# Performance work log

Hardware: AMD Instinct MI355X
Metric: run time of the kernel (lower is better)

The kernel has to match this reference:

```python
import jax, jax.numpy as jnp
import numpy as np

BN_EPS = 1e-5
NEG_SLOPE = 0.2

def _avgpool2(x):
    B, C, H, W = x.shape
    return x.reshape(B, C, H // 2, 2, W // 2, 2).mean(axis=(3, 5))

def _conv1x1(x, w, b):
    # x: [B,C,H,W], w: [O,C], b: [O]
    return jnp.einsum('bchw,oc->bohw', x, w) + b[None, :, None, None]

def _bilinear_resize(x, out_h, out_w):
    # PyTorch F.interpolate(mode='bilinear', align_corners=False) semantics
    B, C, h, w = x.shape
    ys = jnp.maximum((jnp.arange(out_h, dtype=jnp.float32) + 0.5) * (h / out_h) - 0.5, 0.0)
    xs = jnp.maximum((jnp.arange(out_w, dtype=jnp.float32) + 0.5) * (w / out_w) - 0.5, 0.0)
    y0 = jnp.floor(ys).astype(jnp.int32); x0 = jnp.floor(xs).astype(jnp.int32)
    wy = (ys - y0.astype(jnp.float32)).astype(x.dtype)
    wx = (xs - x0.astype(jnp.float32)).astype(x.dtype)
    y1 = jnp.minimum(y0 + 1, h - 1); x1 = jnp.minimum(x0 + 1, w - 1)
    rows = x[:, :, y0, :] * (1.0 - wy)[None, None, :, None] + x[:, :, y1, :] * wy[None, None, :, None]
    out = rows[:, :, :, x0] * (1.0 - wx)[None, None, None, :] + rows[:, :, :, x1] * wx[None, None, None, :]
    return out

def setup_inputs() -> dict:
    key = jax.random.key(0)
    ks = jax.random.split(key, 16)
    B, Cin, Hid, Cout, H, W = 8, 64, 64, 64, 128, 128
    s = 0.05
    return {
        'rgb': jax.random.normal(ks[0], (B, Cin, H, W), dtype=jnp.float32),
        'freq': jax.random.normal(ks[1], (B, Cin, H, W), dtype=jnp.float32),
        'w_q': jax.random.normal(ks[2], (Hid, Cin), dtype=jnp.float32) * s,
        'b_q': jax.random.normal(ks[3], (Hid,), dtype=jnp.float32) * s,
        'w_k': jax.random.normal(ks[4], (Hid, Cin), dtype=jnp.float32) * s,
        'b_k': jax.random.normal(ks[5], (Hid,), dtype=jnp.float32) * s,
        'w_v': jax.random.normal(ks[6], (Hid, Cin), dtype=jnp.float32) * s,
        'b_v': jax.random.normal(ks[7], (Hid,), dtype=jnp.float32) * s,
        'w_o': jax.random.normal(ks[8], (Cout, Hid), dtype=jnp.float32) * s,
        'b_o': jax.random.normal(ks[9], (Cout,), dtype=jnp.float32) * s,
        'bn_gamma': jnp.ones((Cout,), dtype=jnp.float32),
        'bn_beta': jnp.zeros((Cout,), dtype=jnp.float32),
        'bn_mean': jax.random.normal(ks[10], (Cout,), dtype=jnp.float32) * s,
        'bn_var': jax.random.uniform(ks[11], (Cout,), dtype=jnp.float32, minval=0.5, maxval=1.5),
    }

def reference(rgb, freq, w_q, b_q, w_k, b_k, w_v, b_v, w_o, b_o, bn_gamma, bn_beta, bn_mean, bn_var):
    B, C, H, W = rgb.shape
    rgb_ds = _avgpool2(rgb)
    freq_ds = _avgpool2(freq)
    hd, wd = rgb_ds.shape[2], rgb_ds.shape[3]
    hid = w_q.shape[0]
    scale = hid ** (-0.5)
    # 1x1 conv QKV projections, flatten spatial dims to tokens N = hd*wd
    q = _conv1x1(rgb_ds, w_q, b_q).reshape(B, hid, hd * wd)   # [B,hid,N]
    k = _conv1x1(freq_ds, w_k, b_k).reshape(B, hid, hd * wd)  # [B,hid,N]
    v = _conv1x1(freq_ds, w_v, b_v).reshape(B, hid, hd * wd)  # [B,hid,N]
    attn = jax.nn.softmax(jnp.einsum('bcn,bcm->bnm', q, k) * scale, axis=-1)  # [B,N,N]
    z = jnp.einsum('bnm,bcm->bcn', attn, v).reshape(B, hid, hd, wd)
    z = _bilinear_resize(z, H, W)
    y = _conv1x1(z, w_o, b_o)
    # inference-mode BatchNorm fused as affine
    inv = bn_gamma / jnp.sqrt(bn_var + BN_EPS)
    y = (y - bn_mean[None, :, None, None]) * inv[None, :, None, None] + bn_beta[None, :, None, None]
    y = jnp.where(y >= 0, y, NEG_SLOPE * y)  # LeakyReLU(0.2)
    return rgb + y
```

## Files before the change

### kernel.cpp

```cpp
#include <hip/hip_runtime.h>
#include <hip/hip_bf16.h>

typedef unsigned short u16;
typedef unsigned int   u32;
typedef __attribute__((ext_vector_type(8))) short bf16x8;
typedef __attribute__((ext_vector_type(4))) float f32x4;

__device__ __forceinline__ u16 f2bf(float f) {
  u32 u = __float_as_uint(f);
  u32 r = u + 0x7fffu + ((u >> 16) & 1u);
  return (u16)(r >> 16);
}
__device__ __forceinline__ float bflo(u32 u) { return __uint_as_float(u << 16); }
__device__ __forceinline__ float bfhi(u32 u) { return __uint_as_float(u & 0xffff0000u); }
__device__ __forceinline__ u32 packhi(float a, float b) {
  return __builtin_amdgcn_perm(__float_as_uint(b), __float_as_uint(a), 0x07060302u);
}

__global__ __launch_bounds__(256, 4) void k_qkv(
    const float* __restrict__ rgb, const float* __restrict__ freq,
    const float* __restrict__ wq, const float* __restrict__ bq,
    const float* __restrict__ wk, const float* __restrict__ bk,
    const float* __restrict__ wv, const float* __restrict__ bv,
    u16* __restrict__ Qo, u16* __restrict__ Ko, u16* __restrict__ Vo)
{
  __shared__ __align__(16) u16 sm[3 * 4608];
  u16* X  = sm;
  u16* W0 = sm + 4608;
  u16* W1 = sm + 9216;

  const int t    = threadIdx.x;
  const int side = blockIdx.x & 1;
  const int seg  = blockIdx.x >> 1;
  const int idx0 = seg * 64;
  const int bb   = idx0 >> 12;
  const int n0   = idx0 & 4095;
  const int h    = n0 >> 6;
  const float* src = side ? freq : rgb;

  const size_t sbase = (size_t)bb * 64 * 16384 + (size_t)(2 * h) * 128;
  for (int i = 0; i < 2; ++i) {
    int cell = i * 256 + t;
    int tok  = cell & 63;
    int grp  = cell >> 6;
    const float* p0 = src + sbase + 2 * tok + (size_t)(grp * 8) * 16384;
    u32 pk[4];
#pragma unroll
    for (int cc = 0; cc < 8; cc += 2) {
      const float* pa = p0 + (size_t)cc * 16384;
      float2 a0 = *(const float2*)pa;
      float2 a1 = *(const float2*)(pa + 128);
      float v0 = 0.25f * ((a0.x + a0.y) + (a1.x + a1.y));
      const float* pb = pa + 16384;
      float2 b0 = *(const float2*)pb;
      float2 b1 = *(const float2*)(pb + 128);
      float v1 = 0.25f * ((b0.x + b0.y) + (b1.x + b1.y));
      pk[cc >> 1] = (u32)f2bf(v0) | ((u32)f2bf(v1) << 16);
    }
    uint4 q4; q4.x = pk[0]; q4.y = pk[1]; q4.z = pk[2]; q4.w = pk[3];
    *(uint4*)&X[tok * 72 + grp * 8] = q4;
  }
  {
    const int o = t >> 2, c0 = (t & 3) << 4;
    const float4* p4 = (const float4*)((side ? wk : wq) + o * 64 + c0);
    float4 f0 = p4[0], f1 = p4[1], f2 = p4[2], f3 = p4[3];
    uint4 qa, qb;
    qa.x = (u32)f2bf(f0.x) | ((u32)f2bf(f0.y) << 16);
    qa.y = (u32)f2bf(f0.z) | ((u32)f2bf(f0.w) << 16);
    qa.z = (u32)f2bf(f1.x) | ((u32)f2bf(f1.y) << 16);
    qa.w = (u32)f2bf(f1.z) | ((u32)f2bf(f1.w) << 16);
    qb.x = (u32)f2bf(f2.x) | ((u32)f2bf(f2.y) << 16);
    qb.y = (u32)f2bf(f2.z) | ((u32)f2bf(f2.w) << 16);
    qb.z = (u32)f2bf(f3.x) | ((u32)f2bf(f3.y) << 16);
    qb.w = (u32)f2bf(f3.z) | ((u32)f2bf(f3.w) << 16);
    *(uint4*)&W0[o * 72 + c0] = qa;
    *(uint4*)&W0[o * 72 + c0 + 8] = qb;
    if (side) {
      const float4* v4 = (const float4*)(wv + o * 64 + c0);
      float4 g0 = v4[0], g1 = v4[1], g2 = v4[2], g3 = v4[3];
      qa.x = (u32)f2bf(g0.x) | ((u32)f2bf(g0.y) << 16);
      qa.y = (u32)f2bf(g0.z) | ((u32)f2bf(g0.w) << 16);
      qa.z = (u32)f2bf(g1.x) | ((u32)f2bf(g1.y) << 16);
      qa.w = (u32)f2bf(g1.z) | ((u32)f2bf(g1.w) << 16);
      qb.x = (u32)f2bf(g2.x) | ((u32)f2bf(g2.y) << 16);
      qb.y = (u32)f2bf(g2.z) | ((u32)f2bf(g2.w) << 16);
      qb.z = (u32)f2bf(g3.x) | ((u32)f2bf(g3.y) << 16);
      qb.w = (u32)f2bf(g3.z) | ((u32)f2bf(g3.w) << 16);
      *(uint4*)&W1[o * 72 + c0] = qa;
      *(uint4*)&W1[o * 72 + c0 + 8] = qb;
    }
  }
  __syncthreads();

  const int lane = t & 63, w = t >> 6;
  const int l15 = lane & 15, qd = lane >> 4;
  const int tb = w * 16;

  bf16x8 af0 = *(const bf16x8*)&X[(tb + l15) * 72 + qd * 8];
  bf16x8 af1 = *(const bf16x8*)&X[(tb + l15) * 72 + 32 + qd * 8];

  f32x4 acc[4];
#pragma unroll
  for (int nt = 0; nt < 4; ++nt) {
    bf16x8 b0 = *(const bf16x8*)&W0[(nt * 16 + l15) * 72 + qd * 8];
    bf16x8 b1 = *(const bf16x8*)&W0[(nt * 16 + l15) * 72 + 32 + qd * 8];
    f32x4 a = {0.f, 0.f, 0.f, 0.f};
    a = __builtin_amdgcn_mfma_f32_16x16x32_bf16(af0, b0, a, 0, 0, 0);
    a = __builtin_amdgcn_mfma_f32_16x16x32_bf16(af1, b1, a, 0, 0, 0);
    acc[nt] = a;
  }
  {
    const float* bias0 = side ? bk : bq;
    const float sc = side ? 1.f : 0.18033688f;
    u16* dst0 = side ? Ko : Qo;
#pragma unroll
    for (int nt = 0; nt < 4; ++nt) {
      float bia = bias0[nt * 16 + l15];
#pragma unroll
      for (int e = 0; e < 4; ++e) {
        int tok = idx0 + tb + qd * 4 + e;
        dst0[(size_t)tok * 64 + nt * 16 + l15] = f2bf((acc[nt][e] + bia) * sc);
      }
    }
  }

  if (side) {
    f32x4 accv[4];
#pragma unroll
    for (int ct = 0; ct < 4; ++ct) {
      bf16x8 a0 = *(const bf16x8*)&W1[(ct * 16 + l15) * 72 + qd * 8];
      bf16x8 a1 = *(const bf16x8*)&W1[(ct * 16 + l15) * 72 + 32 + qd * 8];
      f32x4 a = {0.f, 0.f, 0.f, 0.f};
      a = __builtin_amdgcn_mfma_f32_16x16x32_bf16(a0, af0, a, 0, 0, 0);
      a = __builtin_amdgcn_mfma_f32_16x16x32_bf16(a1, af1, a, 0, 0, 0);
      accv[ct] = a;
    }
#pragma unroll
    for (int ct = 0; ct < 4; ++ct) {
#pragma unroll
      for (int e = 0; e < 4; ++e) {
        int c = ct * 16 + qd * 4 + e;
        float v = accv[ct][e] + bv[c];
        Vo[((size_t)(bb * 64 + c)) * 4096 + n0 + tb + l15] = f2bf(v);
      }
    }
  }
}

__global__ __launch_bounds__(256, 2) void k_attn(
    const u16* __restrict__ Qg, const u16* __restrict__ Kg,
    const u16* __restrict__ Vg,
    const float* __restrict__ wo, const float* __restrict__ bo,
    const float* __restrict__ gam, const float* __restrict__ bet,
    const float* __restrict__ mean, const float* __restrict__ var,
    u16* __restrict__ Ya)
{
  __shared__ __align__(16) u16 Pb[4 * 4608];
  __shared__ __align__(16) u16 Wl[4608];
  __shared__ __align__(16) u16 Zc[4608];
  __shared__ float lb[256];

  const int b  = blockIdx.x;
  const int q0 = blockIdx.y * 64;
  const int t  = threadIdx.x;
  const int lane = t & 63, w = t >> 6;
  const int l15 = lane & 15, qd = lane >> 4;
  u16* P = Pb + w * 4608;

  {
    const int o = t >> 2, c0 = (t & 3) << 4;
    const float4* p4 = (const float4*)(wo + o * 64 + c0);
    float4 f0 = p4[0], f1 = p4[1], f2 = p4[2], f3 = p4[3];
    uint4 qa, qb;
    qa.x = (u32)f2bf(f0.x) | ((u32)f2bf(f0.y) << 16);
    qa.y = (u32)f2bf(f0.z) | ((u32)f2bf(f0.w) << 16);
    qa.z = (u32)f2bf(f1.x) | ((u32)f2bf(f1.y) << 16);
    qa.w = (u32)f2bf(f1.z) | ((u32)f2bf(f1.w) << 16);
    qb.x = (u32)f2bf(f2.x) | ((u32)f2bf(f2.y) << 16);
    qb.y = (u32)f2bf(f2.z) | ((u32)f2bf(f2.w) << 16);
    qb.z = (u32)f2bf(f3.x) | ((u32)f2bf(f3.y) << 16);
    qb.w = (u32)f2bf(f3.z) | ((u32)f2bf(f3.w) << 16);
    *(uint4*)&Wl[o * 72 + c0] = qa;
    *(uint4*)&Wl[o * 72 + c0 + 8] = qb;
  }

  bf16x8 qf[4][2];
#pragma unroll
  for (int qt = 0; qt < 4; ++qt) {
    const u16* p = Qg + ((size_t)(b * 4096 + q0 + qt * 16 + l15)) * 64 + qd * 8;
    qf[qt][0] = *(const bf16x8*)p;
    qf[qt][1] = *(const bf16x8*)(p + 32);
  }

  f32x4 zacc[4][4];
#pragma unroll
  for (int i = 0; i < 4; ++i)
#pragma unroll
    for (int j = 0; j < 4; ++j) {
      f32x4 z = {0.f, 0.f, 0.f, 0.f};
      zacc[i][j] = z;
    }
  float lacc[4] = {0.f, 0.f, 0.f, 0.f};

  for (int tile = 0; tile < 16; ++tile) {
    const int n0 = w * 1024 + tile * 64;

    bf16x8 kf[4][2], vf[4][2];
#pragma unroll
    for (int mt = 0; mt < 4; ++mt) {
      const u16* p = Kg + ((size_t)(b * 4096 + n0 + mt * 16 + l15)) * 64 + qd * 8;
      kf[mt][0] = *(const bf16x8*)p;
      kf[mt][1] = *(const bf16x8*)(p + 32);
    }
#pragma unroll
    for (int ct = 0; ct < 4; ++ct) {
      const u16* p = Vg + ((size_t)(b * 64 + ct * 16 + l15)) * 4096 + n0 + qd * 8;
      vf[ct][0] = *(const bf16x8*)p;
      vf[ct][1] = *(const bf16x8*)(p + 32);
    }

#pragma unroll
    for (int qt = 0; qt < 4; ++qt) {
#pragma unroll
      for (int mt = 0; mt < 4; ++mt) {
        f32x4 a = {0.f, 0.f, 0.f, 0.f};
        __builtin_amdgcn_s_setprio(1);
        a = __builtin_amdgcn_mfma_f32_16x16x32_bf16(kf[mt][0], qf[qt][0], a, 0, 0, 0);
        a = __builtin_amdgcn_mfma_f32_16x16x32_bf16(kf[mt][1], qf[qt][1], a, 0, 0, 0);
        __builtin_amdgcn_s_setprio(0);
        float p0 = __builtin_amdgcn_exp2f(a[0]);
        float p1 = __builtin_amdgcn_exp2f(a[1]);
        float p2 = __builtin_amdgcn_exp2f(a[2]);
        float p3 = __builtin_amdgcn_exp2f(a[3]);
        lacc[qt] += (p0 + p1) + (p2 + p3);
        uint2 pw;
        pw.x = packhi(p0, p1);
        pw.y = packhi(p2, p3);
        *(uint2*)&P[(qt * 16 + l15) * 72 + mt * 16 + qd * 4] = pw;
      }
    }
#pragma unroll
    for (int qt = 0; qt < 4; ++qt) {
      bf16x8 pf0 = *(const bf16x8*)&P[(qt * 16 + l15) * 72 + qd * 8];
      bf16x8 pf1 = *(const bf16x8*)&P[(qt * 16 + l15) * 72 + 32 + qd * 8];
      __builtin_amdgcn_s_setprio(1);
#pragma unroll
      for (int ct = 0; ct < 4; ++ct) {
        zacc[ct][qt] = __builtin_amdgcn_mfma_f32_16x16x32_bf16(vf[ct][0], pf0, zacc[ct][qt], 0, 0, 0);
        zacc[ct][qt] = __builtin_amdgcn_mfma_f32_16x16x32_bf16(vf[ct][1], pf1, zacc[ct][qt], 0, 0, 0);
      }
      __builtin_amdgcn_s_setprio(0);
    }
  }

#pragma unroll
  for (int qt = 0; qt < 4; ++qt) {
    float l = lacc[qt];
    l += __shfl_xor(l, 16);
    l += __shfl_xor(l, 32);
    lb[w * 64 + qt * 16 + l15] = l;
  }
#pragma unroll
  for (int qt = 0; qt < 4; ++qt)
#pragma unroll
    for (int ct = 0; ct < 4; ++ct) {
      uint2 pw;
      pw.x = packhi(zacc[ct][qt][0], zacc[ct][qt][1]);
      pw.y = packhi(zacc[ct][qt][2], zacc[ct][qt][3]);
      *(uint2*)&P[(qt * 16 + l15) * 72 + ct * 16 + qd * 4] = pw;
    }
  __syncthreads();

  {
    const u32* Pu = (const u32*)Pb;
    u32* Zu = (u32*)Zc;
#pragma unroll
    for (int i = 0; i < 8; ++i) {
      int cell = i * 256 + t;
      int q = cell >> 5, cu = cell & 31;
      float s0 = 0.f, s1 = 0.f;
#pragma unroll
      for (int ww = 0; ww < 4; ++ww) {
        u32 v = Pu[ww * 2304 + q * 36 + cu];
        s0 += bflo(v);
        s1 += bfhi(v);
      }
      float inv = 1.f / (lb[q] + lb[64 + q] + lb[128 + q] + lb[192 + q]);
      Zu[q * 36 + cu] = packhi(s0 * inv, s1 * inv);
    }
  }
  __syncthreads();

  {
    bf16x8 af0 = *(const bf16x8*)&Zc[(w * 16 + l15) * 72 + qd * 8];
    bf16x8 af1 = *(const bf16x8*)&Zc[(w * 16 + l15) * 72 + 32 + qd * 8];
#pragma unroll
    for (int nt = 0; nt < 4; ++nt) {
      bf16x8 b0 = *(const bf16x8*)&Wl[(nt * 16 + l15) * 72 + qd * 8];
      bf16x8 b1 = *(const bf16x8*)&Wl[(nt * 16 + l15) * 72 + 32 + qd * 8];
      f32x4 y = {0.f, 0.f, 0.f, 0.f};
      y = __builtin_amdgcn_mfma_f32_16x16x32_bf16(af0, b0, y, 0, 0, 0);
      y = __builtin_amdgcn_mfma_f32_16x16x32_bf16(af1, b1, y, 0, 0, 0);
      const int o = nt * 16 + l15;
      float A = gam[o] * __frsqrt_rn(var[o] + 1e-5f);
      float B = (bo[o] - mean[o]) * A + bet[o];
#pragma unroll
      for (int e = 0; e < 4; ++e) {
        float v = y[e] * A + B;
        size_t tok = (size_t)(b * 4096 + q0 + w * 16 + qd * 4 + e);
        Ya[tok * 64 + o] = (u16)(__float_as_uint(v) >> 16);
      }
    }
  }
}

__global__ __launch_bounds__(256, 4) void k_out(
    const u16* __restrict__ Ya, const float* __restrict__ rgb,
    float* __restrict__ out)
{
  const int tid = blockIdx.x * 256 + threadIdx.x;
  const int cg  = tid & 1;
  const int px  = tid >> 1;
  const int j = px & 127;
  const int i = (px >> 7) & 127;
  const int b = px >> 14;

  float ys = fmaxf((i + 0.5f) * 0.5f - 0.5f, 0.f);
  int   y0 = (int)ys;
  float wy = ys - (float)y0;
  int   y1 = min(y0 + 1, 63);
  float xs = fmaxf((j + 0.5f) * 0.5f - 0.5f, 0.f);
  int   x0 = (int)xs;
  float wx = xs - (float)x0;
  int   x1 = min(x0 + 1, 63);
  float w00 = (1.f - wy) * (1.f - wx), w01 = (1.f - wy) * wx;
  float w10 = wy * (1.f - wx),         w11 = wy * wx;

  const u16* yb = Ya + (size_t)b * 262144;
  const int b00 = (y0 * 64 + x0) * 64, b01 = (y0 * 64 + x1) * 64;
  const int b10 = (y1 * 64 + x0) * 64, b11 = (y1 * 64 + x1) * 64;
  const int ch0 = cg * 4;

#pragma unroll
  for (int ch = 0; ch < 4; ++ch) {
    const int cc = ch0 + ch;
    uint4 a00 = *(const uint4*)&yb[b00 + cc * 8];
    uint4 a01 = *(const uint4*)&yb[b01 + cc * 8];
    uint4 a10 = *(const uint4*)&yb[b10 + cc * 8];
    uint4 a11 = *(const uint4*)&yb[b11 + cc * 8];
    const u32* u00 = (const u32*)&a00;
    const u32* u01 = (const u32*)&a01;
    const u32* u10 = (const u32*)&a10;
    const u32* u11 = (const u32*)&a11;
#pragma unroll
    for (int e = 0; e < 8; ++e) {
      const int wd = e >> 1;
      float c00 = (e & 1) ? bfhi(u00[wd]) : bflo(u00[wd]);
      float c01 = (e & 1) ? bfhi(u01[wd]) : bflo(u01[wd]);
      float c10 = (e & 1) ? bfhi(u10[wd]) : bflo(u10[wd]);
      float c11 = (e & 1) ? bfhi(u11[wd]) : bflo(u11[wd]);
      float v = w00 * c00 + w01 * c01 + w10 * c10 + w11 * c11;
      v = (v >= 0.f) ? v : 0.2f * v;
      const int o = cc * 8 + e;
      const size_t oi = ((size_t)((b * 64 + o) * 128 + i)) * 128 + j;
      out[oi] = rgb[oi] + v;
    }
  }
}

extern "C" void kernel_launch(void* const* d_in, const int* in_sizes, int n_in,
                              void* d_out, int out_size, void* d_ws, size_t ws_size,
                              hipStream_t stream) {
  (void)in_sizes; (void)n_in; (void)out_size; (void)ws_size;
  const float* rgb  = (const float*)d_in[0];
  const float* freq = (const float*)d_in[1];
  const float* wq   = (const float*)d_in[2];
  const float* bq   = (const float*)d_in[3];
  const float* wk   = (const float*)d_in[4];
  const float* bk   = (const float*)d_in[5];
  const float* wv   = (const float*)d_in[6];
  const float* bv   = (const float*)d_in[7];
  const float* wo   = (const float*)d_in[8];
  const float* bo   = (const float*)d_in[9];
  const float* gam  = (const float*)d_in[10];
  const float* bet  = (const float*)d_in[11];
  const float* mean = (const float*)d_in[12];
  const float* var  = (const float*)d_in[13];

  char* ws = (char*)d_ws;
  u16* Qw = (u16*)(ws);
  u16* Kw = (u16*)(ws + 4194304);
  u16* Vw = (u16*)(ws + 8388608);
  u16* Yw = (u16*)(ws + 12582912);

  k_qkv<<<dim3(1024), dim3(256), 0, stream>>>(rgb, freq, wq, bq, wk, bk, wv, bv,
                                              Qw, Kw, Vw);
  k_attn<<<dim3(8, 64), dim3(256), 0, stream>>>(Qw, Kw, Vw, wo, bo, gam, bet,
                                                mean, var, Yw);
  k_out<<<dim3(1024), dim3(256), 0, stream>>>(Yw, rgb, (float*)d_out);
}
```

Before: 204.2 us.

## Store attention output channel-major and vectorize upsample/residual epilogue

```diff
diff --git a/kernel.cpp b/kernel.cpp
--- a/kernel.cpp
+++ b/kernel.cpp
@@ -39,26 +39,30 @@
   const float* src = side ? freq : rgb;
 
   const size_t sbase = (size_t)bb * 64 * 16384 + (size_t)(2 * h) * 128;
-  for (int i = 0; i < 2; ++i) {
-    int cell = i * 256 + t;
-    int tok  = cell & 63;
-    int grp  = cell >> 6;
-    const float* p0 = src + sbase + 2 * tok + (size_t)(grp * 8) * 16384;
-    u32 pk[4];
-#pragma unroll
-    for (int cc = 0; cc < 8; cc += 2) {
-      const float* pa = p0 + (size_t)cc * 16384;
-      float2 a0 = *(const float2*)pa;
-      float2 a1 = *(const float2*)(pa + 128);
-      float v0 = 0.25f * ((a0.x + a0.y) + (a1.x + a1.y));
+  {
+    const int tokp = t & 31;
+    const int grp  = t >> 5;
+    const float* p0 = src + sbase + 4 * tokp + (size_t)(grp * 8) * 16384;
+    u32 pk0[4], pk1[4];
+#pragma unroll
+    for (int c = 0; c < 8; c += 2) {
+      const float* pa = p0 + (size_t)c * 16384;
+      float4 a0 = *(const float4*)pa;
+      float4 a1 = *(const float4*)(pa + 128);
+      float t0a = 0.25f * ((a0.x + a0.y) + (a1.x + a1.y));
+      float t1a = 0.25f * ((a0.z + a0.w) + (a1.z + a1.w));
       const float* pb = pa + 16384;
-      float2 b0 = *(const float2*)pb;
-      float2 b1 = *(const float2*)(pb + 128);
-      float v1 = 0.25f * ((b0.x + b0.y) + (b1.x + b1.y));
-      pk[cc >> 1] = (u32)f2bf(v0) | ((u32)f2bf(v1) << 16);
-    }
-    uint4 q4; q4.x = pk[0]; q4.y = pk[1]; q4.z = pk[2]; q4.w = pk[3];
-    *(uint4*)&X[tok * 72 + grp * 8] = q4;
+      float4 c0 = *(const float4*)pb;
+      float4 c1 = *(const float4*)(pb + 128);
+      float t0b = 0.25f * ((c0.x + c0.y) + (c1.x + c1.y));
+      float t1b = 0.25f * ((c0.z + c0.w) + (c1.z + c1.w));
+      pk0[c >> 1] = (u32)f2bf(t0a) | ((u32)f2bf(t0b) << 16);
+      pk1[c >> 1] = (u32)f2bf(t1a) | ((u32)f2bf(t1b) << 16);
+    }
+    uint4 qv0; qv0.x = pk0[0]; qv0.y = pk0[1]; qv0.z = pk0[2]; qv0.w = pk0[3];
+    uint4 qv1; qv1.x = pk1[0]; qv1.y = pk1[1]; qv1.z = pk1[2]; qv1.w = pk1[3];
+    *(uint4*)&X[(2 * tokp) * 72 + grp * 8] = qv0;
+    *(uint4*)&X[(2 * tokp + 1) * 72 + grp * 8] = qv1;
   }
   {
     const int o = t >> 2, c0 = (t & 3) << 4;
@@ -159,6 +163,7 @@
   __shared__ __align__(16) u16 Wl[4608];
   __shared__ __align__(16) u16 Zc[4608];
   __shared__ float lb[256];
+  __shared__ float Afs[64], Bfs[64];
 
   const int b  = blockIdx.x;
   const int q0 = blockIdx.y * 64;
@@ -182,6 +187,11 @@
     qb.w = (u32)f2bf(f3.z) | ((u32)f2bf(f3.w) << 16);
     *(uint4*)&Wl[o * 72 + c0] = qa;
     *(uint4*)&Wl[o * 72 + c0 + 8] = qb;
+    if (t < 64) {
+      float A = gam[t] * __frsqrt_rn(var[t] + 1e-5f);
+      Afs[t] = A;
+      Bfs[t] = (bo[t] - mean[t]) * A + bet[t];
+    }
   }
 
   bf16x8 qf[4][2];
@@ -299,73 +309,66 @@
       bf16x8 b0 = *(const bf16x8*)&Wl[(nt * 16 + l15) * 72 + qd * 8];
       bf16x8 b1 = *(const bf16x8*)&Wl[(nt * 16 + l15) * 72 + 32 + qd * 8];
       f32x4 y = {0.f, 0.f, 0.f, 0.f};
-      y = __builtin_amdgcn_mfma_f32_16x16x32_bf16(af0, b0, y, 0, 0, 0);
-      y = __builtin_amdgcn_mfma_f32_16x16x32_bf16(af1, b1, y, 0, 0, 0);
-      const int o = nt * 16 + l15;
-      float A = gam[o] * __frsqrt_rn(var[o] + 1e-5f);
-      float B = (bo[o] - mean[o]) * A + bet[o];
+      y = __builtin_amdgcn_mfma_f32_16x16x32_bf16(b0, af0, y, 0, 0, 0);
+      y = __builtin_amdgcn_mfma_f32_16x16x32_bf16(b1, af1, y, 0, 0, 0);
 #pragma unroll
       for (int e = 0; e < 4; ++e) {
-        float v = y[e] * A + B;
-        size_t tok = (size_t)(b * 4096 + q0 + w * 16 + qd * 4 + e);
-        Ya[tok * 64 + o] = (u16)(__float_as_uint(v) >> 16);
-      }
-    }
-  }
-}
-
-__global__ __launch_bounds__(256, 4) void k_out(
+        const int o = nt * 16 + qd * 4 + e;
+        float v = y[e] * Afs[o] + Bfs[o];
+        Ya[((size_t)(b * 64 + o)) * 4096 + q0 + w * 16 + l15] =
+            (u16)(__float_as_uint(v) >> 16);
+      }
+    }
+  }
+}
+
+__global__ __launch_bounds__(256, 8) void k_out(
     const u16* __restrict__ Ya, const float* __restrict__ rgb,
     float* __restrict__ out)
 {
   const int tid = blockIdx.x * 256 + threadIdx.x;
-  const int cg  = tid & 1;
-  const int px  = tid >> 1;
-  const int j = px & 127;
-  const int i = (px >> 7) & 127;
-  const int b = px >> 14;
-
-  float ys = fmaxf((i + 0.5f) * 0.5f - 0.5f, 0.f);
+  const int g = tid & 31;
+  const int i = (tid >> 5) & 127;
+  const int o = (tid >> 12) & 63;
+  const int b = tid >> 18;
+
+  float ys = fmaxf(0.5f * (float)i - 0.25f, 0.f);
   int   y0 = (int)ys;
   float wy = ys - (float)y0;
   int   y1 = min(y0 + 1, 63);
-  float xs = fmaxf((j + 0.5f) * 0.5f - 0.5f, 0.f);
-  int   x0 = (int)xs;
-  float wx = xs - (float)x0;
-  int   x1 = min(x0 + 1, 63);
-  float w00 = (1.f - wy) * (1.f - wx), w01 = (1.f - wy) * wx;
-  float w10 = wy * (1.f - wx),         w11 = wy * wx;
-
-  const u16* yb = Ya + (size_t)b * 262144;
-  const int b00 = (y0 * 64 + x0) * 64, b01 = (y0 * 64 + x1) * 64;
-  const int b10 = (y1 * 64 + x0) * 64, b11 = (y1 * 64 + x1) * 64;
-  const int ch0 = cg * 4;
-
-#pragma unroll
-  for (int ch = 0; ch < 4; ++ch) {
-    const int cc = ch0 + ch;
-    uint4 a00 = *(const uint4*)&yb[b00 + cc * 8];
-    uint4 a01 = *(const uint4*)&yb[b01 + cc * 8];
-    uint4 a10 = *(const uint4*)&yb[b10 + cc * 8];
-    uint4 a11 = *(const uint4*)&yb[b11 + cc * 8];
-    const u32* u00 = (const u32*)&a00;
-    const u32* u01 = (const u32*)&a01;
-    const u32* u10 = (const u32*)&a10;
-    const u32* u11 = (const u32*)&a11;
-#pragma unroll
-    for (int e = 0; e < 8; ++e) {
-      const int wd = e >> 1;
-      float c00 = (e & 1) ? bfhi(u00[wd]) : bflo(u00[wd]);
-      float c01 = (e & 1) ? bfhi(u01[wd]) : bflo(u01[wd]);
-      float c10 = (e & 1) ? bfhi(u10[wd]) : bflo(u10[wd]);
-      float c11 = (e & 1) ? bfhi(u11[wd]) : bflo(u11[wd]);
-      float v = w00 * c00 + w01 * c01 + w10 * c10 + w11 * c11;
-      v = (v >= 0.f) ? v : 0.2f * v;
-      const int o = cc * 8 + e;
-      const size_t oi = ((size_t)((b * 64 + o) * 128 + i)) * 128 + j;
-      out[oi] = rgb[oi] + v;
-    }
-  }
+
+  const u32* Yw = (const u32*)(Ya + ((size_t)(b * 64 + o)) * 4096);
+  const int base0 = y0 * 32, base1 = y1 * 32;
+  const int gm = (g == 0) ? 0 : g - 1;
+  const int gp = (g == 31) ? 31 : g + 1;
+
+  u32 tm = Yw[base0 + gm], t0 = Yw[base0 + g], tp = Yw[base0 + gp];
+  u32 bm = Yw[base1 + gm], b0w = Yw[base1 + g], bp = Yw[base1 + gp];
+
+  const float iw = 1.f - wy;
+  float r_m1 = iw * bfhi(tm) + wy * bfhi(bm);
+  float r_0  = iw * bflo(t0) + wy * bflo(b0w);
+  float r_1  = iw * bfhi(t0) + wy * bfhi(b0w);
+  float r_2  = iw * bflo(tp) + wy * bflo(bp);
+
+  float v0 = (g == 0)  ? r_0 : 0.25f * r_m1 + 0.75f * r_0;
+  float v1 = 0.75f * r_0 + 0.25f * r_1;
+  float v2 = 0.25f * r_0 + 0.75f * r_1;
+  float v3 = (g == 31) ? r_1 : 0.75f * r_1 + 0.25f * r_2;
+
+  v0 = (v0 >= 0.f) ? v0 : 0.2f * v0;
+  v1 = (v1 >= 0.f) ? v1 : 0.2f * v1;
+  v2 = (v2 >= 0.f) ? v2 : 0.2f * v2;
+  v3 = (v3 >= 0.f) ? v3 : 0.2f * v3;
+
+  const size_t pix = ((size_t)((b * 64 + o) * 128 + i)) * 128 + g * 4;
+  float4 rv = *(const float4*)(rgb + pix);
+  float4 ov;
+  ov.x = rv.x + v0;
+  ov.y = rv.y + v1;
+  ov.z = rv.z + v2;
+  ov.w = rv.w + v3;
+  *(float4*)(out + pix) = ov;
 }
 
 extern "C" void kernel_launch(void* const* d_in, const int* in_sizes, int n_in,
@@ -397,5 +400,5 @@
                                               Qw, Kw, Vw);
   k_attn<<<dim3(8, 64), dim3(256), 0, stream>>>(Qw, Kw, Vw, wo, bo, gam, bet,
                                                 mean, var, Yw);
-  k_out<<<dim3(1024), dim3(256), 0, stream>>>(Yw, rgb, (float*)d_out);
-}
+  k_out<<<dim3(8192), dim3(256), 0, stream>>>(Yw, rgb, (float*)d_out);
+}
```

New measurement: 201.3 us. No clear change (-1.4%).
